# Optimization experiments

Hardware: AMD Instinct MI355X
Metric: run time of the kernel (lower is better)

Reference implementation:

```python
import jax, jax.numpy as jnp
import numpy as np

N_NODES = 100000
N_EDGES = 1600000
D_IN = 256
D_OUT = 256


def _init_linear(key, out_f, in_f):
    # torch nn.Linear default: U(-1/sqrt(in_f), 1/sqrt(in_f))
    kw, kb = jax.random.split(key)
    bound = 1.0 / np.sqrt(in_f)
    W = jax.random.uniform(kw, (out_f, in_f), jnp.float32, -bound, bound)
    b = jax.random.uniform(kb, (out_f,), jnp.float32, -bound, bound)
    return W, b


def setup_inputs() -> dict:
    key = jax.random.key(0)
    ks = jax.random.split(key, 7)
    x = jax.random.normal(ks[0], (N_NODES, D_IN), jnp.float32)
    edge_index = jax.random.randint(ks[1], (2, N_EDGES), 0, N_NODES, jnp.int64)
    W1, b1 = _init_linear(ks[2], D_OUT, D_IN)
    W2, b2 = _init_linear(ks[3], D_OUT // 2, D_OUT)
    W3, b3 = _init_linear(ks[4], D_OUT // 2, D_OUT)
    Wd1, bd1 = _init_linear(ks[5], D_OUT, D_OUT)
    Wd2, bd2 = _init_linear(ks[6], 1, D_OUT)
    return {"x": x, "edge_index": edge_index,
            "W1": W1, "b1": b1, "W2": W2, "b2": b2, "W3": W3, "b3": b3,
            "Wd1": Wd1, "bd1": bd1, "Wd2": Wd2, "bd2": bd2}


def _l2norm(x):
    return x / jnp.linalg.norm(x, axis=-1, keepdims=True)


def reference(x, edge_index, W1, b1, W2, b2, W3, b3, Wd1, bd1, Wd2, bd2):
    src, dst = edge_index[0], edge_index[1]  # source_to_target flow
    x = jax.nn.relu(x @ W1.T + b1)           # [N, D_OUT]
    x = _l2norm(x)
    for _ in range(2):
        # sum-aggregate neighbor messages: scatter-add x[src] into dst
        nm = jax.ops.segment_sum(x[src], dst, num_segments=N_NODES)  # [N, D_OUT]
        x = jax.nn.relu(jnp.concatenate([x @ W2.T + b2, nm @ W3.T + b3], axis=-1))
        x = _l2norm(x)
    x = jax.nn.relu(x @ Wd1.T + bd1)
    return x @ Wd2.T + bd2                    # [N, 1]
```

## Files before the change

### kernel.cpp

```cpp
#include <hip/hip_runtime.h>
#include <math.h>


typedef _Float16 f16x8 __attribute__((ext_vector_type(8)));
typedef float    f32x16 __attribute__((ext_vector_type(16)));

constexpr int DIM = 256;
constexpr int BM  = 128;
constexpr int NBMAX = 392;
constexpr int TB   = 192;

__device__ __forceinline__ unsigned pack_pair(float v) {
    _Float16 hi = (_Float16)v;
    _Float16 lo = (_Float16)(v - (float)hi);
    return (unsigned)__builtin_bit_cast(unsigned short, hi)
         | ((unsigned)__builtin_bit_cast(unsigned short, lo) << 16);
}

__device__ __forceinline__ void glds16(const void* g, void* l) {
    __builtin_amdgcn_global_load_lds(
        (const __attribute__((address_space(1))) unsigned*)g,
        (__attribute__((address_space(3))) unsigned*)l, 16, 0, 0);
}

__global__ __launch_bounds__(256)
void pack_hist_kernel(const float* __restrict__ WA0, const float* __restrict__ WB0,
                      const float* __restrict__ WA1, const float* __restrict__ WB1,
                      const float* __restrict__ WA2, const float* __restrict__ WB2,
                      _Float16* __restrict__ d0, _Float16* __restrict__ d1,
                      _Float16* __restrict__ d2,
                      const int* __restrict__ ei, int E, int nb,
                      int* __restrict__ ghist)
{
    if ((int)blockIdx.x < 192) {
        const int layer = (int)blockIdx.x >> 6;
        const int tid   = ((int)blockIdx.x & 63) * 256 + threadIdx.x;
        const float* WA = layer == 0 ? WA0 : layer == 1 ? WA1 : WA2;
        const float* WB = layer == 0 ? WB0 : layer == 1 ? WB1 : WB2;
        _Float16* dst   = layer == 0 ? d0  : layer == 1 ? d1  : d2;

        const int lane = tid & 63;
        const int frag = tid >> 6;
        const int nt = frag & 7;
        const int ks = (frag >> 3) & 1;
        const int t  = (frag >> 4) & 7;
        const int hl = frag >> 7;
        const int n  = nt * 32 + (lane & 31);
        const int k0 = t * 32 + ks * 16 + (lane >> 5) * 8;
        const float* src = (n < 128) ? &WA[(size_t)n * 256]
                                     : &WB[(size_t)(n - 128) * 256];
        f16x8 o;
        #pragma unroll
        for (int j = 0; j < 8; ++j) {
            const float v = src[k0 + j];
            const _Float16 h = (_Float16)v;
            o[j] = hl ? (_Float16)(v - (float)h) : h;
        }
        *(f16x8*)&dst[(size_t)tid * 8] = o;
    } else {
        __shared__ int h[NBMAX];
        const int tid = threadIdx.x;
        const int b   = (int)blockIdx.x - 192;
        for (int t = tid; t < nb; t += 256) h[t] = 0;
        __syncthreads();
        const int EB = (E + 127) >> 7;
        const int e0 = b * EB, e1 = min(E, e0 + EB);
        for (int e = e0 + tid; e < e1; e += 256)
            atomicAdd(&h[ei[E + e] >> 8], 1);
        __syncthreads();
        for (int t = tid; t < nb; t += 256)
            if (h[t]) atomicAdd(&ghist[t], h[t]);
    }
}

template <int AMODE, int EPI>
__device__ __forceinline__
void gemm2_body(const void* __restrict__ Av, const _Float16* __restrict__ Wpk,
                const float* __restrict__ bA, const float* __restrict__ bB,
                void* __restrict__ outv,
                const float* __restrict__ wd2, const float* __restrict__ bd2,
                float* __restrict__ out1, int M, int bm0)
{
    __shared__ __align__(16) unsigned smem[2][128][32];

    const int tid  = threadIdx.x;
    const int lane = tid & 63;
    const int w    = tid >> 6;
    const int rh   = w >> 1;
    const int ch   = w & 1;
    const int l31  = lane & 31;
    const int lh   = lane >> 5;

    const char* wh_p = (const char*)Wpk + (size_t)(ch * 4 * 64 + lane) * 16;
    const char* wl_p = wh_p + 131072;

    const int srb  = w * 32;
    const int srow = lane >> 3;
    const int scp  = lane & 7;

    f32x16 acc[2][4];
    #pragma unroll
    for (int tr = 0; tr < 2; ++tr)
        #pragma unroll
        for (int tc = 0; tc < 4; ++tc)
            #pragma unroll
            for (int i = 0; i < 16; ++i) acc[tr][tc][i] = 0.0f;

    f16x8 WH0[4], WL0[4], WH1[4], WL1[4];

    auto STAGE = [&](int t, int b) {
        #pragma unroll
        for (int i = 0; i < 4; ++i) {
            const int r  = srb + i * 8 + srow;
            const int rg = min(bm0 + r, M - 1);
            const int cl = scp ^ (r & 7);
            glds16((const char*)Av + (size_t)rg * 1024 + t * 128 + cl * 16,
                   (void*)&smem[b][srb + i * 8][0]);
        }
    };
    auto PW = [&](int s, f16x8* WH, f16x8* WL) {
        #pragma unroll
        for (int tc = 0; tc < 4; ++tc) {
            WH[tc] = *(const f16x8*)(wh_p + (size_t)s * 8192 + tc * 1024);
            WL[tc] = *(const f16x8*)(wl_p + (size_t)s * 8192 + tc * 1024);
        }
    };
    auto LOADA = [&](int b, int ks, f16x8* ah, f16x8* al) {
        #pragma unroll
        for (int tr = 0; tr < 2; ++tr) {
            const int r  = rh * 64 + tr * 32 + l31;
            const int sw = r & 7;
            const int c0 = ks * 4 + lh * 2;
            const unsigned* Ar = &smem[b][r][0];
            const uint4 q0 = *(const uint4*)&Ar[((c0    ) ^ sw) * 4];
            const uint4 q1 = *(const uint4*)&Ar[((c0 + 1) ^ sw) * 4];
            if (AMODE == 1) {
                uint4 uh, ul;
                uh.x = __builtin_amdgcn_perm(q0.y, q0.x, 0x05040100u);
                uh.y = __builtin_amdgcn_perm(q0.w, q0.z, 0x05040100u);
                uh.z = __builtin_amdgcn_perm(q1.y, q1.x, 0x05040100u);
                uh.w = __builtin_amdgcn_perm(q1.w, q1.z, 0x05040100u);
                ul.x = __builtin_amdgcn_perm(q0.y, q0.x, 0x07060302u);
                ul.y = __builtin_amdgcn_perm(q0.w, q0.z, 0x07060302u);
                ul.z = __builtin_amdgcn_perm(q1.y, q1.x, 0x07060302u);
                ul.w = __builtin_amdgcn_perm(q1.w, q1.z, 0x07060302u);
                ah[tr] = __builtin_bit_cast(f16x8, uh);
                al[tr] = __builtin_bit_cast(f16x8, ul);
            } else {
                const float fv[8] = {
                    __builtin_bit_cast(float, q0.x), __builtin_bit_cast(float, q0.y),
                    __builtin_bit_cast(float, q0.z), __builtin_bit_cast(float, q0.w),
                    __builtin_bit_cast(float, q1.x), __builtin_bit_cast(float, q1.y),
                    __builtin_bit_cast(float, q1.z), __builtin_bit_cast(float, q1.w)};
                #pragma unroll
                for (int j = 0; j < 8; ++j) {
                    const _Float16 h = (_Float16)fv[j];
                    ah[tr][j] = h;
                    al[tr][j] = (_Float16)(fv[j] - (float)h);
                }
            }
        }
    };
    auto MF = [&](const f16x8* ah, const f16x8* al,
                  const f16x8* WH, const f16x8* WL) {
        #pragma unroll
        for (int tr = 0; tr < 2; ++tr)
            #pragma unroll
            for (int tc = 0; tc < 4; ++tc) {
                acc[tr][tc] = __builtin_amdgcn_mfma_f32_32x32x16_f16(ah[tr], WH[tc], acc[tr][tc], 0, 0, 0);
                acc[tr][tc] = __builtin_amdgcn_mfma_f32_32x32x16_f16(ah[tr], WL[tc], acc[tr][tc], 0, 0, 0);
                acc[tr][tc] = __builtin_amdgcn_mfma_f32_32x32x16_f16(al[tr], WH[tc], acc[tr][tc], 0, 0, 0);
            }
    };

    STAGE(0, 0);
    PW(0, WH0, WL0);

    #pragma unroll 1
    for (int t = 0; t < 8; ++t) {
        __syncthreads();
        if (t < 7) STAGE(t + 1, (t + 1) & 1);
        const int b = t & 1;
        {
            if (2 * t + 1 < 16) PW(2 * t + 1, WH1, WL1);
            f16x8 ah[2], al[2];
            LOADA(b, 0, ah, al);
            MF(ah, al, WH0, WL0);
        }
        {
            if (2 * t + 2 < 16) PW(2 * t + 2, WH0, WL0);
            f16x8 ah[2], al[2];
            LOADA(b, 1, ah, al);
            MF(ah, al, WH1, WL1);
        }
    }
    __syncthreads();


    if (EPI == 0) {
        float* z = (float*)outv;
        #pragma unroll
        for (int tr = 0; tr < 2; ++tr)
            #pragma unroll
            for (int i = 0; i < 16; ++i) {
                const int r  = rh * 64 + tr * 32 + 4 * lh + (i & 3) + 8 * (i >> 2);
                const int gr = bm0 + r;
                if (gr < M) {
                    #pragma unroll
                    for (int tc = 0; tc < 4; ++tc)
                        z[(size_t)gr * 256 + ch * 128 + tc * 32 + l31] = acc[tr][tc][i];
                }
            }
        return;
    }

    {
        float bias[4];
        #pragma unroll
        for (int tc = 0; tc < 4; ++tc)
            bias[tc] = (ch ? bB : bA)[tc * 32 + l31];
        #pragma unroll
        for (int tr = 0; tr < 2; ++tr)
            #pragma unroll
            for (int tc = 0; tc < 4; ++tc)
                #pragma unroll
                for (int i = 0; i < 16; ++i)
                    acc[tr][tc][i] = fmaxf(acc[tr][tc][i] + bias[tc], 0.0f);
    }

    float* red = (float*)smem;

    if (EPI == 1) {
        float ss[2][16];
        #pragma unroll
        for (int tr = 0; tr < 2; ++tr)
            #pragma unroll
            for (int i = 0; i < 16; ++i) {
                float s = 0.f;
                #pragma unroll
                for (int tc = 0; tc < 4; ++tc) s += acc[tr][tc][i] * acc[tr][tc][i];
                #pragma unroll
                for (int m = 1; m < 32; m <<= 1) s += __shfl_xor(s, m);
                ss[tr][i] = s;
            }
        const int j  = l31;
        const int ji = j & 15, jt = j >> 4;
        red[ch * 128 + rh * 64 + jt * 32 + 4 * lh + (ji & 3) + 8 * (ji >> 2)] = ss[jt][ji];
        __syncthreads();

        unsigned* hp = (unsigned*)outv;
        #pragma unroll
        for (int tr = 0; tr < 2; ++tr)
            #pragma unroll
            for (int i = 0; i < 16; ++i) {
                const int rl = rh * 64 + tr * 32 + 4 * lh + (i & 3) + 8 * (i >> 2);
                const float inv = 1.0f / sqrtf(red[rl] + red[128 + rl]);
                const int gr = bm0 + rl;
                if (gr < M) {
                    #pragma unroll
                    for (int tc = 0; tc < 4; ++tc)
                        hp[(size_t)gr * 256 + ch * 128 + tc * 32 + l31] =
                            pack_pair(acc[tr][tc][i] * inv);
                }
            }
        return;
    }

    {
        float wv[4];
        #pragma unroll
        for (int tc = 0; tc < 4; ++tc) wv[tc] = wd2[ch * 128 + tc * 32 + l31];
        float dd[2][16];
        #pragma unroll
        for (int tr = 0; tr < 2; ++tr)
            #pragma unroll
            for (int i = 0; i < 16; ++i) {
                float s = 0.f;
                #pragma unroll
                for (int tc = 0; tc < 4; ++tc) s += acc[tr][tc][i] * wv[tc];
                #pragma unroll
                for (int m = 1; m < 32; m <<= 1) s += __shfl_xor(s, m);
                dd[tr][i] = s;
            }
        const int j  = l31;
        const int ji = j & 15, jt = j >> 4;
        red[ch * 128 + rh * 64 + jt * 32 + 4 * lh + (ji & 3) + 8 * (ji >> 2)] = dd[jt][ji];
        __syncthreads();
        if (tid < 128) {
            const int gr = bm0 + tid;
            if (gr < M) out1[gr] = red[tid] + red[128 + tid] + bd2[0];
        }
    }
}

__global__ __launch_bounds__(256, 2)
void gemm_l1(const void* __restrict__ Av, const _Float16* __restrict__ wpk,
             const float* __restrict__ bA, const float* __restrict__ bB,
             void* __restrict__ outv, int M,
             const int* __restrict__ ei, int E, int nb,
             int* __restrict__ gcur, int2* __restrict__ ebuf)
{
    if ((int)blockIdx.x >= TB) {
        gemm2_body<0, 1>(Av, wpk, bA, bB, outv, nullptr, nullptr, nullptr, M,
                         ((int)blockIdx.x - TB) * BM);
    } else {
        __shared__ int h[NBMAX], cur[NBMAX];
        const int tid = threadIdx.x;
        const int b   = (int)blockIdx.x;
        for (int t = tid; t < nb; t += 256) h[t] = 0;
        __syncthreads();
        const int EB = (E + TB - 1) / TB;
        const int e0 = b * EB, e1 = min(E, e0 + EB);
        for (int e = e0 + tid; e < e1; e += 256)
            atomicAdd(&h[ei[E + e] >> 8], 1);
        __syncthreads();
        for (int t = tid; t < nb; t += 256)
            cur[t] = atomicAdd(&gcur[t], h[t]);
        __syncthreads();
        for (int e = e0 + tid; e < e1; e += 256) {
            const int d = ei[E + e];
            const int p = atomicAdd(&cur[d >> 8], 1);
            ebuf[p] = make_int2(d, ei[e]);
        }
    }
}

__global__ __launch_bounds__(256, 2)
void gemm_z(const void* __restrict__ Av, const _Float16* __restrict__ wpk,
            void* __restrict__ outv, int M)
{
    gemm2_body<1, 0>(Av, wpk, nullptr, nullptr, outv, nullptr, nullptr, nullptr,
                     M, (int)blockIdx.x * BM);
}

__global__ __launch_bounds__(256, 2)
void gemm_head(const void* __restrict__ Av, const _Float16* __restrict__ wpk,
               const float* __restrict__ bA, const float* __restrict__ bB,
               const float* __restrict__ wd2, const float* __restrict__ bd2,
               float* __restrict__ out1, int M)
{
    gemm2_body<1, 2>(Av, wpk, bA, bB, nullptr, wd2, bd2, out1, M,
                     (int)blockIdx.x * BM);
}


__global__ __launch_bounds__(512)
void scanb_kernel(const int* __restrict__ ghist, int* __restrict__ gboff,
                  int* __restrict__ gcur, int* __restrict__ rp, int M, int E,
                  int nb)
{
    __shared__ int sm[512];
    const int tid = threadIdx.x;
    const int v = (tid < nb) ? ghist[tid] : 0;
    sm[tid] = v;
    __syncthreads();
    for (int off = 1; off < 512; off <<= 1) {
        int t = (tid >= off) ? sm[tid - off] : 0;
        __syncthreads();
        sm[tid] += t;
        __syncthreads();
    }
    if (tid < nb) {
        const int ex = sm[tid] - v;
        gboff[tid] = ex;
        gcur[tid]  = ex;
    }
    if (tid == 0) { gboff[nb] = E; rp[M] = E; }
}

__global__ __launch_bounds__(256)
void bucket_kernel(const int2* __restrict__ ebuf, const int* __restrict__ gboff,
                   int* __restrict__ rp, int* __restrict__ esrc, int M)
{
    const int b   = (int)blockIdx.x;
    const int tid = threadIdx.x;
    const int base = gboff[b], top = gboff[b + 1];
    const int d0 = b << 8;
    __shared__ int c[256], sm[256], cur[256];
    c[tid] = 0;
    __syncthreads();
    for (int j = base + tid; j < top; j += 256)
        atomicAdd(&c[ebuf[j].x - d0], 1);
    __syncthreads();
    sm[tid] = c[tid];
    __syncthreads();
    for (int off = 1; off < 256; off <<= 1) {
        int t = (tid >= off) ? sm[tid - off] : 0;
        __syncthreads();
        sm[tid] += t;
        __syncthreads();
    }
    const int excl = sm[tid] - c[tid];
    const int d = d0 + tid;
    if (d < M) rp[d] = base + excl;
    cur[tid] = base + excl;
    __syncthreads();
    for (int j = base + tid; j < top; j += 256) {
        const int2 e = ebuf[j];
        const int p = atomicAdd(&cur[e.x - d0], 1);
        esrc[p] = e.y;
    }
}

__global__ __launch_bounds__(256)
void fin_kernel(const float* __restrict__ z, const int* __restrict__ rp,
                const int* __restrict__ esrc,
                const float* __restrict__ b2, const float* __restrict__ b3,
                unsigned* __restrict__ hp, int M)
{
    const int v    = blockIdx.x * 4 + (threadIdx.x >> 6);
    const int lane = threadIdx.x & 63;
    if (v >= M) return;
    const int beg = rp[v], end = rp[v + 1];
    const int deg = end - beg;

    const float2 z1 = *(const float2*)&z[(size_t)v * DIM + lane * 2];
    const float2 c2 = *(const float2*)&b2[lane * 2];
    const float2 c3 = *(const float2*)&b3[lane * 2];

    const float* z2 = z + 128;
    float ax0 = 0.f, ay0 = 0.f, ax1 = 0.f, ay1 = 0.f;
    float ax2 = 0.f, ay2 = 0.f, ax3 = 0.f, ay3 = 0.f;

    for (int base = 0; base < deg; base += 64) {
        const int cnt = min(64, deg - base);
        int myidx = 0;
        if (lane < cnt) myidx = esrc[beg + base + lane];
        int j = 0;
        for (; j + 3 < cnt; j += 4) {
            const int s0 = __builtin_amdgcn_readlane(myidx, j);
            const int s1 = __builtin_amdgcn_readlane(myidx, j + 1);
            const int s2 = __builtin_amdgcn_readlane(myidx, j + 2);
            const int s3 = __builtin_amdgcn_readlane(myidx, j + 3);
            const float2 g0 = *(const float2*)&z2[(size_t)s0 * DIM + lane * 2];
            const float2 g1 = *(const float2*)&z2[(size_t)s1 * DIM + lane * 2];
            const float2 g2 = *(const float2*)&z2[(size_t)s2 * DIM + lane * 2];
            const float2 g3 = *(const float2*)&z2[(size_t)s3 * DIM + lane * 2];
            ax0 += g0.x; ay0 += g0.y;
            ax1 += g1.x; ay1 += g1.y;
            ax2 += g2.x; ay2 += g2.y;
            ax3 += g3.x; ay3 += g3.y;
        }
        for (; j < cnt; ++j) {
            const int s0 = __builtin_amdgcn_readlane(myidx, j);
            const float2 g0 = *(const float2*)&z2[(size_t)s0 * DIM + lane * 2];
            ax0 += g0.x; ay0 += g0.y;
        }
    }
    const float sx = (ax0 + ax1) + (ax2 + ax3);
    const float sy = (ay0 + ay1) + (ay2 + ay3);

    const float u1x = fmaxf(z1.x + c2.x, 0.f), u1y = fmaxf(z1.y + c2.y, 0.f);
    const float u2x = fmaxf(sx + c3.x, 0.f),  u2y = fmaxf(sy + c3.y, 0.f);

    float ss = u1x * u1x + u1y * u1y + u2x * u2x + u2y * u2y;
    #pragma unroll
    for (int off = 32; off > 0; off >>= 1) ss += __shfl_xor(ss, off);
    const float inv = 1.0f / sqrtf(ss);

    uint2 p1; p1.x = pack_pair(u1x * inv); p1.y = pack_pair(u1y * inv);
    uint2 p2; p2.x = pack_pair(u2x * inv); p2.y = pack_pair(u2y * inv);
    *(uint2*)&hp[(size_t)v * DIM + lane * 2]       = p1;
    *(uint2*)&hp[(size_t)v * DIM + 128 + lane * 2] = p2;
}


extern "C" void kernel_launch(void* const* d_in, const int* in_sizes, int n_in,
                              void* d_out, int out_size, void* d_ws, size_t ws_size,
                              hipStream_t stream)
{
    const float* x   = (const float*)d_in[0];
    const int*   ei  = (const int*)d_in[1];
    const float* W1  = (const float*)d_in[2];
    const float* b1  = (const float*)d_in[3];
    const float* W2  = (const float*)d_in[4];
    const float* b2  = (const float*)d_in[5];
    const float* W3  = (const float*)d_in[6];
    const float* b3  = (const float*)d_in[7];
    const float* Wd1 = (const float*)d_in[8];
    const float* bd1 = (const float*)d_in[9];
    const float* Wd2 = (const float*)d_in[10];
    const float* bd2 = (const float*)d_in[11];
    float* out = (float*)d_out;

    const int M = in_sizes[0] / DIM;
    const int E = in_sizes[1] / 2;
    const int nb = (M + 255) >> 8;

    unsigned* hp  = (unsigned*)d_ws;
    float*    z   = (float*)(hp + (size_t)M * DIM);
    int*   rp     = (int*)(z + (size_t)M * DIM);
    int*   esrc   = rp + (M + 1);
    int*   ghist  = esrc + E;
    int*   gboff  = ghist + nb;
    int*   gcur   = gboff + nb + 1;
    int2*  ebuf   = (int2*)z;

    size_t woff = (size_t)((char*)(gcur + nb) - (char*)d_ws);
    woff = (woff + 255) & ~(size_t)255;
    _Float16* wpk1 = (_Float16*)((char*)d_ws + woff);
    _Float16* wpk2 = wpk1 + 131072;
    _Float16* wpkd = wpk2 + 131072;

    hipMemsetAsync(ghist, 0, sizeof(int) * nb, stream);

    const int gb  = (M + BM - 1) / BM;
    const int fb  = (M + 3) / 4;

    pack_hist_kernel<<<320, 256, 0, stream>>>(
        W1, W1 + 128 * DIM, W2, W3, Wd1, Wd1 + 128 * DIM, wpk1, wpk2, wpkd,
        ei, E, nb, ghist);

    scanb_kernel<<<1, 512, 0, stream>>>(ghist, gboff, gcur, rp, M, E, nb);

    gemm_l1<<<TB + gb, 256, 0, stream>>>(
        x, wpk1, b1, b1 + 128, hp, M, ei, E, nb, gcur, ebuf);

    bucket_kernel<<<nb, 256, 0, stream>>>(ebuf, gboff, rp, esrc, M);

    gemm_z<<<gb, 256, 0, stream>>>(hp, wpk2, z, M);
    fin_kernel<<<fb, 256, 0, stream>>>(z, rp, esrc, b2, b3, hp, M);

    gemm_z<<<gb, 256, 0, stream>>>(hp, wpk2, z, M);
    fin_kernel<<<fb, 256, 0, stream>>>(z, rp, esrc, b2, b3, hp, M);

    gemm_head<<<gb, 256, 0, stream>>>(
        hp, wpkd, bd1, bd1 + 128, Wd2, bd2, out, M);
}
```

Before: 712.2 us.

## Stage GEMM epilogue stores through LDS and use nontemporal accesses in gather kernel

The GEMM epilogue for raw and normalized outputs now writes accumulator fragments into shared memory in four 32-row passes, then stores whole rows to global memory as 16-byte vector writes instead of scattered 4-byte writes. The fin kernel marks its self-feature load, edge-index load and packed output stores as nontemporal so streaming data is less likely to evict the gathered neighbor rows from cache. The staging adds extra barriers and LDS traffic per tile, and nontemporal hints may hurt if that data is reused soon.

```diff
diff --git a/kernel.cpp b/kernel.cpp
--- a/kernel.cpp
+++ b/kernel.cpp
@@ -21,6 +21,12 @@
     __builtin_amdgcn_global_load_lds(
         (const __attribute__((address_space(1))) unsigned*)g,
         (__attribute__((address_space(3))) unsigned*)l, 16, 0, 0);
+}
+
+__device__ __forceinline__ float2 ntld_f2(const float* p) {
+    unsigned long long v =
+        __builtin_nontemporal_load((const unsigned long long*)p);
+    return __builtin_bit_cast(float2, v);
 }
 
 __global__ __launch_bounds__(256)
@@ -197,24 +203,9 @@
     __syncthreads();
 
 
-    if (EPI == 0) {
-        float* z = (float*)outv;
-        #pragma unroll
-        for (int tr = 0; tr < 2; ++tr)
-            #pragma unroll
-            for (int i = 0; i < 16; ++i) {
-                const int r  = rh * 64 + tr * 32 + 4 * lh + (i & 3) + 8 * (i >> 2);
-                const int gr = bm0 + r;
-                if (gr < M) {
-                    #pragma unroll
-                    for (int tc = 0; tc < 4; ++tc)
-                        z[(size_t)gr * 256 + ch * 128 + tc * 32 + l31] = acc[tr][tc][i];
-                }
-            }
-        return;
-    }
-
-    {
+    float* red = (float*)smem;
+
+    if (EPI != 0) {
         float bias[4];
         #pragma unroll
         for (int tc = 0; tc < 4; ++tc)
@@ -227,8 +218,6 @@
                 for (int i = 0; i < 16; ++i)
                     acc[tr][tc][i] = fmaxf(acc[tr][tc][i] + bias[tc], 0.0f);
     }
-
-    float* red = (float*)smem;
 
     if (EPI == 1) {
         float ss[2][16];
@@ -247,22 +236,48 @@
         const int ji = j & 15, jt = j >> 4;
         red[ch * 128 + rh * 64 + jt * 32 + 4 * lh + (ji & 3) + 8 * (ji >> 2)] = ss[jt][ji];
         __syncthreads();
-
-        unsigned* hp = (unsigned*)outv;
         #pragma unroll
         for (int tr = 0; tr < 2; ++tr)
             #pragma unroll
             for (int i = 0; i < 16; ++i) {
                 const int rl = rh * 64 + tr * 32 + 4 * lh + (i & 3) + 8 * (i >> 2);
                 const float inv = 1.0f / sqrtf(red[rl] + red[128 + rl]);
-                const int gr = bm0 + rl;
-                if (gr < M) {
+                #pragma unroll
+                for (int tc = 0; tc < 4; ++tc)
+                    acc[tr][tc][i] = __builtin_bit_cast(float,
+                        pack_pair(acc[tr][tc][i] * inv));
+            }
+    }
+
+    if (EPI == 0 || EPI == 1) {
+        float* lds = (float*)smem;
+        unsigned* outu = (unsigned*)outv;
+        #pragma unroll
+        for (int p = 0; p < 4; ++p) {
+            __syncthreads();
+            if (rh == (p >> 1)) {
+                const int tr = p & 1;
+                #pragma unroll
+                for (int i = 0; i < 16; ++i) {
+                    const int ro = 4 * lh + (i & 3) + 8 * (i >> 2);
                     #pragma unroll
                     for (int tc = 0; tc < 4; ++tc)
-                        hp[(size_t)gr * 256 + ch * 128 + tc * 32 + l31] =
-                            pack_pair(acc[tr][tc][i] * inv);
+                        lds[ro * 256 + ch * 128 + tc * 32 + l31] =
+                            (EPI == 0) ? acc[tr][tc][i] : acc[tr][tc][i];
                 }
             }
+            __syncthreads();
+            const unsigned* ldsu = (const unsigned*)lds;
+            #pragma unroll
+            for (int k = 0; k < 8; ++k) {
+                const int flat = k * 1024 + tid * 4;
+                const int gr   = bm0 + p * 32 + (flat >> 8);
+                if (gr < M) {
+                    uint4 v = *(const uint4*)&ldsu[flat];
+                    *(uint4*)&outu[(size_t)(bm0 + p * 32) * 256 + flat] = v;
+                }
+            }
+        }
         return;
     }
 
@@ -414,7 +429,7 @@
     const int beg = rp[v], end = rp[v + 1];
     const int deg = end - beg;
 
-    const float2 z1 = *(const float2*)&z[(size_t)v * DIM + lane * 2];
+    const float2 z1 = ntld_f2(&z[(size_t)v * DIM + lane * 2]);
     const float2 c2 = *(const float2*)&b2[lane * 2];
     const float2 c3 = *(const float2*)&b3[lane * 2];
 
@@ -425,7 +440,8 @@
     for (int base = 0; base < deg; base += 64) {
         const int cnt = min(64, deg - base);
         int myidx = 0;
-        if (lane < cnt) myidx = esrc[beg + base + lane];
+        if (lane < cnt)
+            myidx = __builtin_nontemporal_load(&esrc[beg + base + lane]);
         int j = 0;
         for (; j + 3 < cnt; j += 4) {
             const int s0 = __builtin_amdgcn_readlane(myidx, j);
@@ -460,8 +476,12 @@
 
     uint2 p1; p1.x = pack_pair(u1x * inv); p1.y = pack_pair(u1y * inv);
     uint2 p2; p2.x = pack_pair(u2x * inv); p2.y = pack_pair(u2y * inv);
-    *(uint2*)&hp[(size_t)v * DIM + lane * 2]       = p1;
-    *(uint2*)&hp[(size_t)v * DIM + 128 + lane * 2] = p2;
+    __builtin_nontemporal_store(
+        __builtin_bit_cast(unsigned long long, p1),
+        (unsigned long long*)&hp[(size_t)v * DIM + lane * 2]);
+    __builtin_nontemporal_store(
+        __builtin_bit_cast(unsigned long long, p2),
+        (unsigned long long*)&hp[(size_t)v * DIM + 128 + lane * 2]);
 }
 
 
```

Measured after the change: 702.5 us. About the same (-1.4%).
